# Optimization experiments

Hardware: AMD Instinct MI355X
Metric: run time of the kernel (lower is better)

## Reference

```python
import jax, jax.numpy as jnp
import numpy as np
import math

EPS = 1e-5
BN_SCALE = 1.0 / math.sqrt(1.0 + EPS)  # eval BatchNorm with running mean 0, var 1


def _ln(x, g, b):
    m = jnp.mean(x, axis=-1, keepdims=True)
    v = jnp.mean((x - m) ** 2, axis=-1, keepdims=True)
    return (x - m) * jax.lax.rsqrt(v + EPS) * g + b


def _swish(x):
    return x * jax.nn.sigmoid(x)


def _ffn(x, ng, nb, w1, b1, w2, b2):
    h = _ln(x, ng, nb)
    h = _swish(h @ w1.T + b1)
    return h @ w2.T + b2


def _mhsa(x, a_ng, a_nb, qkv_w, qkv_b, rel_w, out_w, out_b):
    B, T, D = x.shape
    H, hd = rel_w.shape  # rel_pos_proj: Linear(head_dim, num_heads), weight [H, hd]
    h = _ln(x, a_ng, a_nb)
    qkv = (h @ qkv_w.T + qkv_b).reshape(B, T, 3, H, hd)
    q = qkv[:, :, 0].transpose(0, 2, 1, 3)  # [B,H,T,hd]
    k = qkv[:, :, 1].transpose(0, 2, 1, 3)
    v = qkv[:, :, 2].transpose(0, 2, 1, 3)
    scores = jnp.einsum('bhqd,bhkd->bhqk', q, k) * (hd ** -0.5)
    # relative sinusoidal PE over 2T-1 offsets
    pos = jnp.arange(-(T - 1), T, dtype=x.dtype)[:, None]
    div = jnp.exp(jnp.arange(0, hd, 2, dtype=x.dtype) * (-math.log(10000.0) / hd))
    ang = pos * div  # [2T-1, hd/2]
    pe = jnp.zeros((2 * T - 1, hd), dtype=x.dtype)
    pe = pe.at[:, 0::2].set(jnp.sin(ang)).at[:, 1::2].set(jnp.cos(ang))
    rel_bias = pe @ rel_w.T  # [2T-1, H]
    idx = jnp.arange(T)[:, None] - jnp.arange(T)[None, :] + (T - 1)  # [T,T]
    bias = rel_bias[idx].transpose(2, 0, 1)  # [H,T,T]
    attn = jax.nn.softmax(scores + bias[None], axis=-1)
    o = jnp.einsum('bhqk,bhkd->bhqd', attn, v).transpose(0, 2, 1, 3).reshape(B, T, D)
    return o @ out_w.T + out_b


def _conv(x, c_ng, c_nb, pw1_w, pw1_b, dw_w, dw_b, bn_g, bn_b, pw2_w, pw2_b):
    B, T, D = x.shape
    K = dw_w.shape[1]
    h = _ln(x, c_ng, c_nb)
    h = h @ pw1_w.T + pw1_b  # pointwise conv == linear, [B,T,2D]
    a, g = jnp.split(h, 2, axis=-1)
    h = a * jax.nn.sigmoid(g)  # GLU, [B,T,D]
    h = h.transpose(0, 2, 1)  # [B,D,T]
    h = jax.lax.conv_general_dilated(
        h, dw_w[:, None, :], window_strides=(1,), padding=[(K // 2, K // 2)],
        dimension_numbers=('NCH', 'OIH', 'NCH'), feature_group_count=D) + dw_b[:, None]
    h = h * (BN_SCALE * bn_g)[:, None] + bn_b[:, None]  # eval-mode BatchNorm1d
    h = _swish(h)
    h = h.transpose(0, 2, 1)  # [B,T,D]
    return h @ pw2_w.T + pw2_b


def _forward(x, g_ffn1, b_ffn1, g_mhsa, b_mhsa, g_conv, b_conv, g_ffn2, b_ffn2, g_out, b_out,
             f1_ng, f1_nb, f1_w1, f1_b1, f1_w2, f1_b2,
             f2_ng, f2_nb, f2_w1, f2_b1, f2_w2, f2_b2,
             a_ng, a_nb, qkv_w, qkv_b, rel_w, out_w, out_b,
             c_ng, c_nb, pw1_w, pw1_b, dw_w, dw_b, bn_g, bn_b, pw2_w, pw2_b):
    x = x + 0.5 * _ffn(_ln(x, g_ffn1, b_ffn1), f1_ng, f1_nb, f1_w1, f1_b1, f1_w2, f1_b2)
    x = x + _mhsa(_ln(x, g_mhsa, b_mhsa), a_ng, a_nb, qkv_w, qkv_b, rel_w, out_w, out_b)
    x = x + _conv(_ln(x, g_conv, b_conv), c_ng, c_nb, pw1_w, pw1_b, dw_w, dw_b, bn_g, bn_b, pw2_w, pw2_b)
    x = _ln(x + 0.5 * _ffn(_ln(x, g_ffn2, b_ffn2), f2_ng, f2_nb, f2_w1, f2_b1, f2_w2, f2_b2), g_out, b_out)
    return x


def setup_inputs() -> dict:
    key = jax.random.key(0)
    B, T, D, H, F, K = 8, 2048, 256, 4, 1024, 31
    ks = iter(jax.random.split(key, 16))
    w = lambda shape, s: jax.random.normal(next(ks), shape, jnp.float32) * s
    d = {}
    d['x'] = w((B, T, D), 1.0)
    for n in ['g_ffn1', 'g_mhsa', 'g_conv', 'g_ffn2', 'g_out', 'f1_ng', 'f2_ng', 'a_ng', 'c_ng', 'bn_g']:
        d[n] = jnp.ones((D,), jnp.float32)
    for n in ['b_ffn1', 'b_mhsa', 'b_conv', 'b_ffn2', 'b_out', 'f1_nb', 'f2_nb', 'a_nb', 'c_nb', 'bn_b']:
        d[n] = jnp.zeros((D,), jnp.float32)
    d['f1_w1'] = w((F, D), 0.05); d['f1_b1'] = jnp.zeros((F,), jnp.float32)
    d['f1_w2'] = w((D, F), 0.03); d['f1_b2'] = jnp.zeros((D,), jnp.float32)
    d['f2_w1'] = w((F, D), 0.05); d['f2_b1'] = jnp.zeros((F,), jnp.float32)
    d['f2_w2'] = w((D, F), 0.03); d['f2_b2'] = jnp.zeros((D,), jnp.float32)
    d['qkv_w'] = w((3 * D, D), 0.05); d['qkv_b'] = jnp.zeros((3 * D,), jnp.float32)
    d['rel_w'] = w((H, D // H), 0.05)
    d['out_w'] = w((D, D), 0.05); d['out_b'] = jnp.zeros((D,), jnp.float32)
    d['pw1_w'] = w((2 * D, D), 0.05); d['pw1_b'] = jnp.zeros((2 * D,), jnp.float32)
    d['dw_w'] = w((D, K), 0.1); d['dw_b'] = jnp.zeros((D,), jnp.float32)
    d['pw2_w'] = w((D, D), 0.05); d['pw2_b'] = jnp.zeros((D,), jnp.float32)
    return d


def reference(x, g_ffn1, b_ffn1, g_mhsa, b_mhsa, g_conv, b_conv, g_ffn2, b_ffn2, g_out, b_out,
              f1_ng, f1_nb, f1_w1, f1_b1, f1_w2, f1_b2,
              f2_ng, f2_nb, f2_w1, f2_b1, f2_w2, f2_b2,
              a_ng, a_nb, qkv_w, qkv_b, rel_w, out_w, out_b,
              c_ng, c_nb, pw1_w, pw1_b, dw_w, dw_b, bn_g, bn_b, pw2_w, pw2_b):
    return _forward(x, g_ffn1, b_ffn1, g_mhsa, b_mhsa, g_conv, b_conv, g_ffn2, b_ffn2, g_out, b_out,
                    f1_ng, f1_nb, f1_w1, f1_b1, f1_w2, f1_b2,
                    f2_ng, f2_nb, f2_w1, f2_b1, f2_w2, f2_b2,
                    a_ng, a_nb, qkv_w, qkv_b, rel_w, out_w, out_b,
                    c_ng, c_nb, pw1_w, pw1_b, dw_w, dw_b, bn_g, bn_b, pw2_w, pw2_b)
```

## Files before the change

kernel.cpp:

```cpp
#include <hip/hip_runtime.h>
#include <math.h>


typedef _Float16 half8 __attribute__((ext_vector_type(8)));
typedef _Float16 half4v __attribute__((ext_vector_type(4)));
typedef float floatx4 __attribute__((ext_vector_type(4)));

#define LN_EPS 1e-5f
#define BN_SCALE 0.9999950000374996f
#define LOG2E 1.44269504f
#define QSCALE (0.125f * LOG2E)

__device__ __forceinline__ void async_copy16(const _Float16* g, _Float16* l) {
    __builtin_amdgcn_global_load_lds(
        (const __attribute__((address_space(1))) void*)g,
        (__attribute__((address_space(3))) void*)l, 16, 0, 0);
}

struct CastJobs { const float* s[7]; _Float16* d[7]; };
__global__ __launch_bounds__(256) void cast_all(CastJobs j) {
    int i = blockIdx.x * 256 + threadIdx.x;
    int seg, base;
    if (i < 1048576)      { seg = i >> 18; base = seg << 18; }
    else if (i < 1245184) { seg = 4; base = 1048576; }
    else if (i < 1310720) { seg = 5; base = 1245184; }
    else                  { seg = 6; base = 1310720; }
    j.d[seg][i - base] = (_Float16)j.s[seg][i - base];
}

__global__ __launch_bounds__(256) void cast_pw1_kernel(const float* __restrict__ w,
        const float* __restrict__ b, _Float16* __restrict__ wp, float* __restrict__ bp) {
    int i = blockIdx.x * 256 + threadIdx.x;
    int p = i >> 8, c = i & 255;
    int chunk = p >> 4, within = p & 15;
    int orig = ((chunk & 1) ? 256 : 0) + (chunk >> 1) * 16 + within;
    wp[i] = (_Float16)w[orig * 256 + c];
    if (c == 0) bp[p] = b[orig];
}

__global__ __launch_bounds__(256) void ln2_kernel(const float* __restrict__ x,
        const float* __restrict__ g1, const float* __restrict__ b1,
        const float* __restrict__ g2, const float* __restrict__ b2,
        _Float16* __restrict__ y) {
    int wave = threadIdx.x >> 6, lane = threadIdx.x & 63;
    size_t row = (size_t)blockIdx.x * 4 + wave;
    float4 v = ((const float4*)(x + row * 256))[lane];
    float s = v.x + v.y + v.z + v.w;
    float s2 = v.x * v.x + v.y * v.y + v.z * v.z + v.w * v.w;
    #pragma unroll
    for (int m = 1; m < 64; m <<= 1) { s += __shfl_xor(s, m, 64); s2 += __shfl_xor(s2, m, 64); }
    float mean = s * (1.f / 256.f);
    float var = s2 * (1.f / 256.f) - mean * mean;
    float rs = rsqrtf(var + LN_EPS);
    int c0 = lane * 4;
    float y0 = (v.x - mean) * rs * g1[c0 + 0] + b1[c0 + 0];
    float y1 = (v.y - mean) * rs * g1[c0 + 1] + b1[c0 + 1];
    float y2 = (v.z - mean) * rs * g1[c0 + 2] + b1[c0 + 2];
    float y3 = (v.w - mean) * rs * g1[c0 + 3] + b1[c0 + 3];
    float t = y0 + y1 + y2 + y3;
    float t2 = y0 * y0 + y1 * y1 + y2 * y2 + y3 * y3;
    #pragma unroll
    for (int m = 1; m < 64; m <<= 1) { t += __shfl_xor(t, m, 64); t2 += __shfl_xor(t2, m, 64); }
    float mean2 = t * (1.f / 256.f);
    float var2 = t2 * (1.f / 256.f) - mean2 * mean2;
    float rs2 = rsqrtf(var2 + LN_EPS);
    half4v o;
    o[0] = (_Float16)((y0 - mean2) * rs2 * g2[c0 + 0] + b2[c0 + 0]);
    o[1] = (_Float16)((y1 - mean2) * rs2 * g2[c0 + 1] + b2[c0 + 1]);
    o[2] = (_Float16)((y2 - mean2) * rs2 * g2[c0 + 2] + b2[c0 + 2]);
    o[3] = (_Float16)((y3 - mean2) * rs2 * g2[c0 + 3] + b2[c0 + 3]);
    *(half4v*)(y + row * 256 + c0) = o;
}

template <int EPI>
__global__ __launch_bounds__(256) void gemm128(
        const _Float16* __restrict__ A, const _Float16* __restrict__ W,
        const float* __restrict__ bias, _Float16* __restrict__ outh,
        _Float16* __restrict__ outv, int N, int K) {
    __shared__ _Float16 As[128 * 64];
    __shared__ _Float16 Ws[128 * 64];
    int tid = threadIdx.x, wave = tid >> 6, lane = tid & 63;
    int n0 = blockIdx.x * 128, m0 = blockIdx.y * 128;
    int wr = wave >> 1, wc = wave & 1;
    floatx4 acc[4][4] = {};
    int l15 = lane & 15, quad = lane >> 4;
    int srow = wave * 32 + (lane >> 3);
    int scg  = (lane & 7) ^ ((lane >> 3) & 7);
    const _Float16* Aptr = A + (size_t)(m0 + srow) * K + scg * 8;
    const _Float16* Wptr = W + (size_t)(n0 + srow) * K + scg * 8;
    _Float16* AsBase = As + wave * 32 * 64;
    _Float16* WsBase = Ws + wave * 32 * 64;
    int r7 = l15 & 7;
    for (int k0 = 0; k0 < K; k0 += 64) {
        __syncthreads();
        #pragma unroll
        for (int i = 0; i < 4; i++)
            async_copy16(Aptr + k0 + (size_t)i * 8 * K, AsBase + i * 8 * 64);
        #pragma unroll
        for (int i = 0; i < 4; i++)
            async_copy16(Wptr + k0 + (size_t)i * 8 * K, WsBase + i * 8 * 64);
        __syncthreads();
        #pragma unroll
        for (int ks = 0; ks < 2; ks++) {
            int cg = ((ks * 4 + quad) ^ r7) * 8;
            half8 a[4], b[4];
            #pragma unroll
            for (int i = 0; i < 4; i++)
                a[i] = *(const half8*)&As[(wr * 64 + i * 16 + l15) * 64 + cg];
            #pragma unroll
            for (int j = 0; j < 4; j++)
                b[j] = *(const half8*)&Ws[(wc * 64 + j * 16 + l15) * 64 + cg];
            #pragma unroll
            for (int i = 0; i < 4; i++)
                #pragma unroll
                for (int j = 0; j < 4; j++)
                    acc[i][j] = __builtin_amdgcn_mfma_f32_16x16x32_f16(a[i], b[j], acc[i][j], 0, 0, 0);
        }
    }
    #pragma unroll
    for (int i = 0; i < 4; i++) {
        int mrow = m0 + wr * 64 + i * 16 + quad * 4;
        if (EPI == 2) {
            #pragma unroll
            for (int jp = 0; jp < 2; jp++) {
                int j = 2 * jp;
                int Pa = n0 + wc * 64 + j * 16 + l15;
                float ba = bias[Pa], bg = bias[Pa + 16];
                int d = ((Pa >> 5) << 4) + l15;
                #pragma unroll
                for (int r = 0; r < 4; r++) {
                    float av = acc[i][j][r] + ba;
                    float gv = acc[i][j + 1][r] + bg;
                    outh[(size_t)(mrow + r) * 256 + d] = (_Float16)(av / (1.f + __expf(-gv)));
                }
            }
        } else if (EPI == 5) {
            float qs = (n0 < 256) ? QSCALE : 1.f;
            #pragma unroll
            for (int j = 0; j < 4; j++) {
                int n = n0 + wc * 64 + j * 16 + l15;
                float bv = bias[n];
                if (n0 < 512) {
                    #pragma unroll
                    for (int r = 0; r < 4; r++)
                        outh[(size_t)(mrow + r) * N + n] = (_Float16)((acc[i][j][r] + bv) * qs);
                } else {
                    int hv = (n - 512) >> 6, d = (n - 512) & 63;
                    int bb = m0 >> 11;
                    int t0 = (m0 & 2047) + wr * 64 + i * 16 + quad * 4;
                    half4v vv;
                    #pragma unroll
                    for (int r = 0; r < 4; r++) vv[r] = (_Float16)(acc[i][j][r] + bv);
                    *(half4v*)(outv + ((size_t)((bb * 4 + hv) * 64 + d)) * 2048 + t0) = vv;
                }
            }
        } else {
            #pragma unroll
            for (int j = 0; j < 4; j++) {
                int n = n0 + wc * 64 + j * 16 + l15;
                float bv = bias[n];
                #pragma unroll
                for (int r = 0; r < 4; r++) {
                    float c = acc[i][j][r] + bv;
                    outh[(size_t)(mrow + r) * N + n] = (_Float16)(c / (1.f + __expf(-c)));
                }
            }
        }
    }
}

template <int FIN>
__global__ __launch_bounds__(256) void gemm_row(
        const _Float16* __restrict__ A, const _Float16* __restrict__ W,
        const float* __restrict__ bias, const float* __restrict__ res, float alpha,
        float* __restrict__ xNext, _Float16* __restrict__ t16out,
        float* __restrict__ finalOut,
        const float* __restrict__ g1, const float* __restrict__ b1,
        const float* __restrict__ g2, const float* __restrict__ b2, int K) {
    __shared__ _Float16 As[64 * 64];
    __shared__ _Float16 Ws[256 * 64];
    __shared__ float red[4][64][2];
    int tid = threadIdx.x, wave = tid >> 6, lane = tid & 63;
    int l15 = lane & 15, quad = lane >> 4;
    int m0 = blockIdx.x * 64;
    int sgsw = (tid & 7) ^ ((tid >> 3) & 7);
    int r7 = l15 & 7;
    floatx4 acc[4][4] = {};
    for (int k0 = 0; k0 < K; k0 += 64) {
        __syncthreads();
        #pragma unroll
        for (int i = 0; i < 2; i++) {
            int idx = tid + 256 * i;
            async_copy16(A + (size_t)(m0 + (idx >> 3)) * K + k0 + sgsw * 8, As + idx * 8);
        }
        #pragma unroll
        for (int i = 0; i < 8; i++) {
            int idx = tid + 256 * i;
            async_copy16(W + (size_t)(idx >> 3) * K + k0 + sgsw * 8, Ws + idx * 8);
        }
        __syncthreads();
        #pragma unroll
        for (int ks = 0; ks < 2; ks++) {
            int cg = ((ks * 4 + quad) ^ r7) * 8;
            half8 a[4], b[4];
            #pragma unroll
            for (int i = 0; i < 4; i++)
                a[i] = *(const half8*)&As[(i * 16 + l15) * 64 + cg];
            #pragma unroll
            for (int j = 0; j < 4; j++)
                b[j] = *(const half8*)&Ws[(wave * 64 + j * 16 + l15) * 64 + cg];
            #pragma unroll
            for (int i = 0; i < 4; i++)
                #pragma unroll
                for (int j = 0; j < 4; j++)
                    acc[i][j] = __builtin_amdgcn_mfma_f32_16x16x32_f16(a[i], b[j], acc[i][j], 0, 0, 0);
        }
    }
    int col[4];
    float bv[4], gg1[4], bb1[4], gg2[4], bb2[4];
    #pragma unroll
    for (int j = 0; j < 4; j++) {
        col[j] = wave * 64 + j * 16 + l15;
        bv[j] = bias[col[j]];
        gg1[j] = g1[col[j]]; bb1[j] = b1[col[j]];
        if (FIN == 0) { gg2[j] = g2[col[j]]; bb2[j] = b2[col[j]]; }
    }
    #pragma unroll
    for (int i = 0; i < 4; i++)
        #pragma unroll
        for (int r = 0; r < 4; r++) {
            size_t m = m0 + i * 16 + quad * 4 + r;
            #pragma unroll
            for (int j = 0; j < 4; j++) {
                float xv = res[m * 256 + col[j]] + alpha * (acc[i][j][r] + bv[j]);
                acc[i][j][r] = xv;
                if (FIN == 0) xNext[m * 256 + col[j]] = xv;
            }
        }
    #pragma unroll
    for (int i = 0; i < 4; i++)
        #pragma unroll
        for (int r = 0; r < 4; r++) {
            float s1 = 0.f, s2 = 0.f;
            #pragma unroll
            for (int j = 0; j < 4; j++) { float v = acc[i][j][r]; s1 += v; s2 += v * v; }
            #pragma unroll
            for (int mm = 1; mm < 16; mm <<= 1) { s1 += __shfl_xor(s1, mm, 64); s2 += __shfl_xor(s2, mm, 64); }
            if (l15 == 0) { red[wave][i * 16 + quad * 4 + r][0] = s1; red[wave][i * 16 + quad * 4 + r][1] = s2; }
        }
    __syncthreads();
    float mean1[4][4], rs1[4][4];
    #pragma unroll
    for (int i = 0; i < 4; i++)
        #pragma unroll
        for (int r = 0; r < 4; r++) {
            int row = i * 16 + quad * 4 + r;
            float T1 = red[0][row][0] + red[1][row][0] + red[2][row][0] + red[3][row][0];
            float T2 = red[0][row][1] + red[1][row][1] + red[2][row][1] + red[3][row][1];
            float mn = T1 * (1.f / 256.f);
            mean1[i][r] = mn;
            rs1[i][r] = rsqrtf(T2 * (1.f / 256.f) - mn * mn + LN_EPS);
        }
    if (FIN == 1) {
        #pragma unroll
        for (int i = 0; i < 4; i++)
            #pragma unroll
            for (int r = 0; r < 4; r++) {
                size_t m = m0 + i * 16 + quad * 4 + r;
                #pragma unroll
                for (int j = 0; j < 4; j++)
                    finalOut[m * 256 + col[j]] =
                        (acc[i][j][r] - mean1[i][r]) * rs1[i][r] * gg1[j] + bb1[j];
            }
        return;
    }
    #pragma unroll
    for (int i = 0; i < 4; i++)
        #pragma unroll
        for (int r = 0; r < 4; r++)
            #pragma unroll
            for (int j = 0; j < 4; j++)
                acc[i][j][r] = (acc[i][j][r] - mean1[i][r]) * rs1[i][r] * gg1[j] + bb1[j];
    __syncthreads();
    #pragma unroll
    for (int i = 0; i < 4; i++)
        #pragma unroll
        for (int r = 0; r < 4; r++) {
            float s1 = 0.f, s2 = 0.f;
            #pragma unroll
            for (int j = 0; j < 4; j++) { float v = acc[i][j][r]; s1 += v; s2 += v * v; }
            #pragma unroll
            for (int mm = 1; mm < 16; mm <<= 1) { s1 += __shfl_xor(s1, mm, 64); s2 += __shfl_xor(s2, mm, 64); }
            if (l15 == 0) { red[wave][i * 16 + quad * 4 + r][0] = s1; red[wave][i * 16 + quad * 4 + r][1] = s2; }
        }
    __syncthreads();
    #pragma unroll
    for (int i = 0; i < 4; i++)
        #pragma unroll
        for (int r = 0; r < 4; r++) {
            int row = i * 16 + quad * 4 + r;
            float T1 = red[0][row][0] + red[1][row][0] + red[2][row][0] + red[3][row][0];
            float T2 = red[0][row][1] + red[1][row][1] + red[2][row][1] + red[3][row][1];
            float mn = T1 * (1.f / 256.f);
            float rs = rsqrtf(T2 * (1.f / 256.f) - mn * mn + LN_EPS);
            size_t m = m0 + row;
            #pragma unroll
            for (int j = 0; j < 4; j++)
                t16out[m * 256 + col[j]] =
                    (_Float16)((acc[i][j][r] - mn) * rs * gg2[j] + bb2[j]);
        }
}

__global__ __launch_bounds__(256) void relbias_kernel(const float* __restrict__ rel_w,
                                                      float* __restrict__ rb) {
    int i = blockIdx.x * 256 + threadIdx.x;
    if (i >= 4095 * 4) return;
    int p = i >> 2, h = i & 3;
    float pos = (float)(p - 2047);
    const float c = -logf(10000.f) / 64.f;
    float acc = 0.f;
    for (int k = 0; k < 32; k++) {
        float dv = expf((float)(2 * k) * c);
        float ang = pos * dv;
        acc += sinf(ang) * rel_w[h * 64 + 2 * k] + cosf(ang) * rel_w[h * 64 + 2 * k + 1];
    }
    rb[h * 4095 + p] = acc * LOG2E;
}

__global__ __launch_bounds__(256) void attn_kernel(const _Float16* __restrict__ qkv,
        const _Float16* __restrict__ vtg, const float* __restrict__ rb,
        float* __restrict__ opart, float* __restrict__ lpart) {
    const int T = 2048;
    int qt = blockIdx.x & 15, ksp = blockIdx.x >> 4, h = blockIdx.y, b = blockIdx.z;
    int tid = threadIdx.x, wave = tid >> 6, lane = tid & 63;
    __shared__ __align__(16) _Float16 PQ[128 * 72];
    __shared__ __align__(16) _Float16 Ks[64][72];
    __shared__ __align__(16) _Float16 Vt[64][72];
    __shared__ __align__(16) float bias4[4][192];
    auto Qs = (_Float16(*)[72])PQ;
    auto Ps = (_Float16(*)[32][72])PQ;

    int l15 = lane & 15, quad = lane >> 4, kq = quad * 8;
    size_t qrow0 = (size_t)b * T + qt * 128;
    #pragma unroll
    for (int i = 0; i < 4; i++) {
        int idx = tid + 256 * i, r = idx >> 3, sg = idx & 7;
        *(float4*)(&Qs[r][sg * 8]) = *(const float4*)(qkv + (qrow0 + r) * 768 + h * 64 + sg * 8);
    }
    __syncthreads();
    half8 qa[2][2];
    #pragma unroll
    for (int u = 0; u < 2; u++)
        #pragma unroll
        for (int ks = 0; ks < 2; ks++)
            qa[u][ks] = *(const half8*)(&Qs[u * 64 + wave * 16 + l15][ks * 32 + kq]);
    half8 ones;
    #pragma unroll
    for (int j = 0; j < 8; j++) ones[j] = (_Float16)1.f;

    floatx4 oacc[2][4] = {};
    floatx4 lacc[2] = {};
    const float* rbh = rb + h * 4095;
    const _Float16* vbase = vtg + ((size_t)(b * 4 + h)) * 64 * 2048;
    const _Float16* kbase = qkv + ((size_t)b * T) * 768 + 256 + h * 64;
    int cshift = (63 - l15) & 3;

    for (int kt = ksp * 16; kt < ksp * 16 + 16; kt++) {
        __syncthreads();
        #pragma unroll
        for (int i = 0; i < 2; i++) {
            int idx = tid + 256 * i, r = idx >> 3, sg = idx & 7;
            *(float4*)(&Ks[r][sg * 8]) = *(const float4*)(kbase + (size_t)(kt * 64 + r) * 768 + sg * 8);
            *(float4*)(&Vt[r][sg * 8]) = *(const float4*)(vbase + (size_t)r * 2048 + kt * 64 + sg * 8);
        }
        if (tid < 192) {
            int base = qt * 128 - kt * 64 + 1984;
            float v = rbh[min(base + tid, 4094)];
            #pragma unroll
            for (int c = 0; c < 4; c++) {
                int idx = tid - c;
                if (idx >= 0) bias4[c][idx] = v;
            }
        }
        __syncthreads();
        half8 kf[2][4];
        #pragma unroll
        for (int ks = 0; ks < 2; ks++)
            #pragma unroll
            for (int nt = 0; nt < 4; nt++)
                kf[ks][nt] = *(const half8*)(&Ks[nt * 16 + l15][ks * 32 + kq]);
        floatx4 s[2][4];
        #pragma unroll
        for (int u = 0; u < 2; u++)
            #pragma unroll
            for (int nt = 0; nt < 4; nt++) {
                int cb = u * 64 + wave * 16 + quad * 4 - (nt * 16 + l15) + 63;
                s[u][nt] = *(const floatx4*)&bias4[cshift][cb - cshift];
            }
        #pragma unroll
        for (int u = 0; u < 2; u++)
            #pragma unroll
            for (int ks = 0; ks < 2; ks++)
                #pragma unroll
                for (int nt = 0; nt < 4; nt++)
                    s[u][nt] = __builtin_amdgcn_mfma_f32_16x16x32_f16(qa[u][ks], kf[ks][nt], s[u][nt], 0, 0, 0);
        #pragma unroll
        for (int u = 0; u < 2; u++)
            #pragma unroll
            for (int nt = 0; nt < 4; nt++)
                #pragma unroll
                for (int r = 0; r < 4; r++)
                    Ps[wave][u * 16 + quad * 4 + r][nt * 16 + l15] =
                        (_Float16)__builtin_amdgcn_exp2f(fminf(s[u][nt][r], 15.86f));
        half8 vf[2][4];
        #pragma unroll
        for (int ks = 0; ks < 2; ks++)
            #pragma unroll
            for (int nt = 0; nt < 4; nt++)
                vf[ks][nt] = *(const half8*)(&Vt[nt * 16 + l15][ks * 32 + kq]);
        #pragma unroll
        for (int u = 0; u < 2; u++)
            #pragma unroll
            for (int ks = 0; ks < 2; ks++) {
                half8 pa = *(const half8*)(&Ps[wave][u * 16 + l15][ks * 32 + kq]);
                lacc[u] = __builtin_amdgcn_mfma_f32_16x16x32_f16(pa, ones, lacc[u], 0, 0, 0);
                #pragma unroll
                for (int nt = 0; nt < 4; nt++)
                    oacc[u][nt] = __builtin_amdgcn_mfma_f32_16x16x32_f16(pa, vf[ks][nt], oacc[u][nt], 0, 0, 0);
            }
    }
    float* obase = opart + (size_t)ksp * 16384 * 256;
    #pragma unroll
    for (int u = 0; u < 2; u++) {
        size_t orow0 = qrow0 + u * 64 + wave * 16 + quad * 4;
        #pragma unroll
        for (int r = 0; r < 4; r++)
            #pragma unroll
            for (int nt = 0; nt < 4; nt++)
                obase[(orow0 + r) * 256 + h * 64 + nt * 16 + l15] = oacc[u][nt][r];
        if (l15 == 0) {
            int q = qt * 128 + u * 64 + wave * 16 + quad * 4;
            float* lp = lpart + ksp * 65536 + ((b * 4 + h) << 11) + q;
            #pragma unroll
            for (int r = 0; r < 4; r++) lp[r] = lacc[u][r];
        }
    }
}

__global__ __launch_bounds__(256) void attn_combine(const float* __restrict__ opart,
        const float* __restrict__ lpart, _Float16* __restrict__ o16) {
    int wave = threadIdx.x >> 6, lane = threadIdx.x & 63;
    size_t row = (size_t)blockIdx.x * 4 + wave;
    int c0 = lane * 4;
    float4 a = ((const float4*)(opart + row * 256))[lane];
    float4 bq = ((const float4*)(opart + (size_t)16384 * 256 + row * 256))[lane];
    int b = (int)(row >> 11), q = (int)(row & 2047), h = c0 >> 6;
    int li = ((b * 4 + h) << 11) + q;
    float inv = 1.f / (lpart[li] + lpart[65536 + li]);
    half4v o;
    o[0] = (_Float16)((a.x + bq.x) * inv);
    o[1] = (_Float16)((a.y + bq.y) * inv);
    o[2] = (_Float16)((a.z + bq.z) * inv);
    o[3] = (_Float16)((a.w + bq.w) * inv);
    *(half4v*)(o16 + row * 256 + c0) = o;
}

__global__ __launch_bounds__(256) void dwconv_kernel(const _Float16* __restrict__ glu,
        const float* __restrict__ dw_w, const float* __restrict__ dw_b,
        const float* __restrict__ bn_g, const float* __restrict__ bn_b,
        _Float16* __restrict__ out) {
    const int T = 2048;
    int d = threadIdx.x;
    int b = blockIdx.y, t0 = blockIdx.x * 32;
    const _Float16* base = glu + ((size_t)b * T) * 256 + d;
    float w[31], win[31];
    #pragma unroll
    for (int j = 0; j < 31; j++) w[j] = dw_w[d * 31 + j];
    #pragma unroll
    for (int j = 0; j < 31; j++) {
        int tt = t0 - 15 + j;
        win[j] = (tt >= 0 && tt < T) ? (float)base[(size_t)tt * 256] : 0.f;
    }
    float dwb = dw_b[d];
    float bns = BN_SCALE * bn_g[d];
    float bnb = bn_b[d];
    size_t orow = ((size_t)b * T) * 256 + d;
    #pragma unroll
    for (int i = 0; i < 32; i += 4) {
        float nl[4];
        #pragma unroll
        for (int u = 0; u < 4; u++) {
            int tn = t0 + i + u + 16;
            nl[u] = (tn < T) ? (float)base[(size_t)tn * 256] : 0.f;
        }
        #pragma unroll
        for (int u = 0; u < 4; u++) {
            int t = t0 + i + u;
            float acc = dwb;
            #pragma unroll
            for (int j = 0; j < 31; j++) acc += win[j] * w[j];
            float bn = acc * bns + bnb;
            out[orow + (size_t)t * 256] = (_Float16)(bn / (1.f + __expf(-bn)));
            #pragma unroll
            for (int j = 0; j < 30; j++) win[j] = win[j + 1];
            win[30] = nl[u];
        }
    }
}

extern "C" void kernel_launch(void* const* d_in, const int* in_sizes, int n_in,
                              void* d_out, int out_size, void* d_ws, size_t ws_size,
                              hipStream_t stream) {
    (void)in_sizes; (void)n_in; (void)out_size; (void)ws_size;
    const float* x      = (const float*)d_in[0];
    const float* g_ffn1 = (const float*)d_in[1];
    const float* g_mhsa = (const float*)d_in[2];
    const float* g_conv = (const float*)d_in[3];
    const float* g_ffn2 = (const float*)d_in[4];
    const float* g_out  = (const float*)d_in[5];
    const float* f1_ng  = (const float*)d_in[6];
    const float* f2_ng  = (const float*)d_in[7];
    const float* a_ng   = (const float*)d_in[8];
    const float* c_ng   = (const float*)d_in[9];
    const float* bn_g   = (const float*)d_in[10];
    const float* b_ffn1 = (const float*)d_in[11];
    const float* b_mhsa = (const float*)d_in[12];
    const float* b_conv = (const float*)d_in[13];
    const float* b_ffn2 = (const float*)d_in[14];
    const float* b_out  = (const float*)d_in[15];
    const float* f1_nb  = (const float*)d_in[16];
    const float* f2_nb  = (const float*)d_in[17];
    const float* a_nb   = (const float*)d_in[18];
    const float* c_nb   = (const float*)d_in[19];
    const float* bn_b   = (const float*)d_in[20];
    const float* f1_w1  = (const float*)d_in[21];
    const float* f1_b1  = (const float*)d_in[22];
    const float* f1_w2  = (const float*)d_in[23];
    const float* f1_b2  = (const float*)d_in[24];
    const float* f2_w1  = (const float*)d_in[25];
    const float* f2_b1  = (const float*)d_in[26];
    const float* f2_w2  = (const float*)d_in[27];
    const float* f2_b2  = (const float*)d_in[28];
    const float* qkv_w  = (const float*)d_in[29];
    const float* qkv_b  = (const float*)d_in[30];
    const float* rel_w  = (const float*)d_in[31];
    const float* out_w  = (const float*)d_in[32];
    const float* out_b  = (const float*)d_in[33];
    const float* pw1_w  = (const float*)d_in[34];
    const float* pw1_b  = (const float*)d_in[35];
    const float* dw_w   = (const float*)d_in[36];
    const float* dw_b   = (const float*)d_in[37];
    const float* pw2_w  = (const float*)d_in[38];
    const float* pw2_b  = (const float*)d_in[39];

    const int BT = 16384;
    char* ws = (char*)d_ws;
    size_t off = 0;
    auto alloc = [&](size_t bytes) -> char* {
        char* p = ws + off;
        off += (bytes + 255) & ~(size_t)255;
        return p;
    };
    _Float16* wf1w1 = (_Float16*)alloc(262144 * 2);
    _Float16* wf1w2 = (_Float16*)alloc(262144 * 2);
    _Float16* wf2w1 = (_Float16*)alloc(262144 * 2);
    _Float16* wf2w2 = (_Float16*)alloc(262144 * 2);
    _Float16* wqkv  = (_Float16*)alloc(196608 * 2);
    _Float16* wout  = (_Float16*)alloc(65536 * 2);
    _Float16* wpw1  = (_Float16*)alloc(131072 * 2);
    float* pb1      = (float*)alloc(512 * 4);
    _Float16* wpw2  = (_Float16*)alloc(65536 * 2);
    float* rbbuf    = (float*)alloc(4 * 4095 * 4);
    float* xA       = (float*)alloc((size_t)BT * 256 * 4);
    float* xB       = (float*)alloc((size_t)BT * 256 * 4);
    _Float16* t16   = (_Float16*)alloc((size_t)BT * 256 * 2);
    char* R1        = alloc((size_t)BT * 1024 * 2);
    _Float16* vtg   = (_Float16*)alloc((size_t)8 * 4 * 64 * 2048 * 2);
    float* opart    = (float*)alloc((size_t)2 * BT * 256 * 4);
    float* lpart    = (float*)alloc((size_t)2 * 65536 * 4);
    _Float16* glu16 = (_Float16*)alloc((size_t)BT * 256 * 2);
    _Float16* c16   = (_Float16*)alloc((size_t)BT * 256 * 2);
    _Float16* o16   = (_Float16*)alloc((size_t)BT * 256 * 2);
    _Float16* h16   = (_Float16*)R1;
    _Float16* qkv16 = (_Float16*)R1;

    CastJobs cj;
    cj.s[0] = f1_w1; cj.d[0] = wf1w1;
    cj.s[1] = f1_w2; cj.d[1] = wf1w2;
    cj.s[2] = f2_w1; cj.d[2] = wf2w1;
    cj.s[3] = f2_w2; cj.d[3] = wf2w2;
    cj.s[4] = qkv_w; cj.d[4] = wqkv;
    cj.s[5] = out_w; cj.d[5] = wout;
    cj.s[6] = pw2_w; cj.d[6] = wpw2;
    cast_all<<<5376, 256, 0, stream>>>(cj);
    cast_pw1_kernel<<<512, 256, 0, stream>>>(pw1_w, pw1_b, wpw1, pb1);
    relbias_kernel<<<64, 256, 0, stream>>>(rel_w, rbbuf);

    ln2_kernel<<<BT / 4, 256, 0, stream>>>(x, g_ffn1, b_ffn1, f1_ng, f1_nb, t16);
    gemm128<1><<<dim3(8, 128), 256, 0, stream>>>(t16, wf1w1, f1_b1, h16, nullptr, 1024, 256);
    gemm_row<0><<<256, 256, 0, stream>>>(h16, wf1w2, f1_b2, x, 0.5f, xA, t16, nullptr,
                                         g_mhsa, b_mhsa, a_ng, a_nb, 1024);
    gemm128<5><<<dim3(6, 128), 256, 0, stream>>>(t16, wqkv, qkv_b, qkv16, vtg, 768, 256);
    attn_kernel<<<dim3(32, 4, 8), 256, 0, stream>>>(qkv16, vtg, rbbuf, opart, lpart);
    attn_combine<<<BT / 4, 256, 0, stream>>>(opart, lpart, o16);
    gemm_row<0><<<256, 256, 0, stream>>>(o16, wout, out_b, xA, 1.f, xB, t16, nullptr,
                                         g_conv, b_conv, c_ng, c_nb, 256);
    gemm128<2><<<dim3(4, 128), 256, 0, stream>>>(t16, wpw1, pb1, glu16, nullptr, 512, 256);
    dwconv_kernel<<<dim3(64, 8), 256, 0, stream>>>(glu16, dw_w, dw_b, bn_g, bn_b, c16);
    gemm_row<0><<<256, 256, 0, stream>>>(c16, wpw2, pw2_b, xB, 1.f, xA, t16, nullptr,
                                         g_ffn2, b_ffn2, f2_ng, f2_nb, 256);
    gemm128<1><<<dim3(8, 128), 256, 0, stream>>>(t16, wf2w1, f2_b1, h16, nullptr, 1024, 256);
    gemm_row<1><<<256, 256, 0, stream>>>(h16, wf2w2, f2_b2, xA, 0.5f, nullptr, nullptr,
                                         (float*)d_out, g_out, b_out, nullptr, nullptr, 1024);
}
```

Before: 486.4 us.

## Drop attention split-K combine, shrink row-GEMM tiles to 32 rows

The attention kernel no longer splits the key range into two partial passes written as fp32 partials and merged by a separate combine kernel. Each block now owns 64 queries over all 2048 keys and writes normalized fp16 output directly, and K/V/Q tiles are loaded with async global-to-LDS copies. The LayerNorm-fused row GEMM goes from 64-row to 32-row tiles, doubling its grid to 512 blocks for better CU occupancy. The trade-offs are more redundant weight-tile loads per row in the GEMM and a longer serial key loop per attention block, plus an unpadded LDS layout that may cause bank conflicts.

```diff
diff --git a/kernel.cpp b/kernel.cpp
--- a/kernel.cpp
+++ b/kernel.cpp
@@ -177,22 +177,18 @@
         float* __restrict__ finalOut,
         const float* __restrict__ g1, const float* __restrict__ b1,
         const float* __restrict__ g2, const float* __restrict__ b2, int K) {
-    __shared__ _Float16 As[64 * 64];
+    __shared__ _Float16 As[32 * 64];
     __shared__ _Float16 Ws[256 * 64];
-    __shared__ float red[4][64][2];
+    __shared__ float red[4][32][2];
     int tid = threadIdx.x, wave = tid >> 6, lane = tid & 63;
     int l15 = lane & 15, quad = lane >> 4;
-    int m0 = blockIdx.x * 64;
+    int m0 = blockIdx.x * 32;
     int sgsw = (tid & 7) ^ ((tid >> 3) & 7);
     int r7 = l15 & 7;
-    floatx4 acc[4][4] = {};
+    floatx4 acc[2][4] = {};
     for (int k0 = 0; k0 < K; k0 += 64) {
         __syncthreads();
-        #pragma unroll
-        for (int i = 0; i < 2; i++) {
-            int idx = tid + 256 * i;
-            async_copy16(A + (size_t)(m0 + (idx >> 3)) * K + k0 + sgsw * 8, As + idx * 8);
-        }
+        async_copy16(A + (size_t)(m0 + (tid >> 3)) * K + k0 + sgsw * 8, As + tid * 8);
         #pragma unroll
         for (int i = 0; i < 8; i++) {
             int idx = tid + 256 * i;
@@ -202,15 +198,15 @@
         #pragma unroll
         for (int ks = 0; ks < 2; ks++) {
             int cg = ((ks * 4 + quad) ^ r7) * 8;
-            half8 a[4], b[4];
-            #pragma unroll
-            for (int i = 0; i < 4; i++)
+            half8 a[2], b[4];
+            #pragma unroll
+            for (int i = 0; i < 2; i++)
                 a[i] = *(const half8*)&As[(i * 16 + l15) * 64 + cg];
             #pragma unroll
             for (int j = 0; j < 4; j++)
                 b[j] = *(const half8*)&Ws[(wave * 64 + j * 16 + l15) * 64 + cg];
             #pragma unroll
-            for (int i = 0; i < 4; i++)
+            for (int i = 0; i < 2; i++)
                 #pragma unroll
                 for (int j = 0; j < 4; j++)
                     acc[i][j] = __builtin_amdgcn_mfma_f32_16x16x32_f16(a[i], b[j], acc[i][j], 0, 0, 0);
@@ -226,7 +222,7 @@
         if (FIN == 0) { gg2[j] = g2[col[j]]; bb2[j] = b2[col[j]]; }
     }
     #pragma unroll
-    for (int i = 0; i < 4; i++)
+    for (int i = 0; i < 2; i++)
         #pragma unroll
         for (int r = 0; r < 4; r++) {
             size_t m = m0 + i * 16 + quad * 4 + r;
@@ -238,7 +234,7 @@
             }
         }
     #pragma unroll
-    for (int i = 0; i < 4; i++)
+    for (int i = 0; i < 2; i++)
         #pragma unroll
         for (int r = 0; r < 4; r++) {
             float s1 = 0.f, s2 = 0.f;
@@ -249,9 +245,9 @@
             if (l15 == 0) { red[wave][i * 16 + quad * 4 + r][0] = s1; red[wave][i * 16 + quad * 4 + r][1] = s2; }
         }
     __syncthreads();
-    float mean1[4][4], rs1[4][4];
-    #pragma unroll
-    for (int i = 0; i < 4; i++)
+    float mean1[2][4], rs1[2][4];
+    #pragma unroll
+    for (int i = 0; i < 2; i++)
         #pragma unroll
         for (int r = 0; r < 4; r++) {
             int row = i * 16 + quad * 4 + r;
@@ -263,7 +259,7 @@
         }
     if (FIN == 1) {
         #pragma unroll
-        for (int i = 0; i < 4; i++)
+        for (int i = 0; i < 2; i++)
             #pragma unroll
             for (int r = 0; r < 4; r++) {
                 size_t m = m0 + i * 16 + quad * 4 + r;
@@ -275,7 +271,7 @@
         return;
     }
     #pragma unroll
-    for (int i = 0; i < 4; i++)
+    for (int i = 0; i < 2; i++)
         #pragma unroll
         for (int r = 0; r < 4; r++)
             #pragma unroll
@@ -283,7 +279,7 @@
                 acc[i][j][r] = (acc[i][j][r] - mean1[i][r]) * rs1[i][r] * gg1[j] + bb1[j];
     __syncthreads();
     #pragma unroll
-    for (int i = 0; i < 4; i++)
+    for (int i = 0; i < 2; i++)
         #pragma unroll
         for (int r = 0; r < 4; r++) {
             float s1 = 0.f, s2 = 0.f;
@@ -295,7 +291,7 @@
         }
     __syncthreads();
     #pragma unroll
-    for (int i = 0; i < 4; i++)
+    for (int i = 0; i < 2; i++)
         #pragma unroll
         for (int r = 0; r < 4; r++) {
             int row = i * 16 + quad * 4 + r;
@@ -329,52 +325,50 @@
 
 __global__ __launch_bounds__(256) void attn_kernel(const _Float16* __restrict__ qkv,
         const _Float16* __restrict__ vtg, const float* __restrict__ rb,
-        float* __restrict__ opart, float* __restrict__ lpart) {
+        _Float16* __restrict__ o16) {
     const int T = 2048;
-    int qt = blockIdx.x & 15, ksp = blockIdx.x >> 4, h = blockIdx.y, b = blockIdx.z;
+    int qt = blockIdx.x, h = blockIdx.y, b = blockIdx.z;
     int tid = threadIdx.x, wave = tid >> 6, lane = tid & 63;
-    __shared__ __align__(16) _Float16 PQ[128 * 72];
-    __shared__ __align__(16) _Float16 Ks[64][72];
-    __shared__ __align__(16) _Float16 Vt[64][72];
-    __shared__ __align__(16) float bias4[4][192];
-    auto Qs = (_Float16(*)[72])PQ;
-    auto Ps = (_Float16(*)[32][72])PQ;
+    __shared__ __align__(16) _Float16 PQ[4608];
+    __shared__ __align__(16) _Float16 Ks[64 * 64];
+    __shared__ __align__(16) _Float16 Vt[64 * 64];
+    __shared__ __align__(16) float bias4[4][136];
+    _Float16* Qs = PQ;
+    auto Ps = (_Float16(*)[16][72])PQ;
 
     int l15 = lane & 15, quad = lane >> 4, kq = quad * 8;
-    size_t qrow0 = (size_t)b * T + qt * 128;
-    #pragma unroll
-    for (int i = 0; i < 4; i++) {
-        int idx = tid + 256 * i, r = idx >> 3, sg = idx & 7;
-        *(float4*)(&Qs[r][sg * 8]) = *(const float4*)(qkv + (qrow0 + r) * 768 + h * 64 + sg * 8);
+    size_t qrow0 = (size_t)b * T + qt * 64;
+    #pragma unroll
+    for (int i = 0; i < 2; i++) {
+        int idx = tid + 256 * i;
+        async_copy16(qkv + (qrow0 + (idx >> 3)) * 768 + h * 64 + (idx & 7) * 8, PQ + idx * 8);
     }
     __syncthreads();
-    half8 qa[2][2];
-    #pragma unroll
-    for (int u = 0; u < 2; u++)
-        #pragma unroll
-        for (int ks = 0; ks < 2; ks++)
-            qa[u][ks] = *(const half8*)(&Qs[u * 64 + wave * 16 + l15][ks * 32 + kq]);
+    half8 qa[2];
+    #pragma unroll
+    for (int ks = 0; ks < 2; ks++)
+        qa[ks] = *(const half8*)&Qs[(wave * 16 + l15) * 64 + ks * 32 + kq];
     half8 ones;
     #pragma unroll
     for (int j = 0; j < 8; j++) ones[j] = (_Float16)1.f;
 
-    floatx4 oacc[2][4] = {};
-    floatx4 lacc[2] = {};
+    floatx4 oacc[4] = {};
+    floatx4 lacc = {};
     const float* rbh = rb + h * 4095;
     const _Float16* vbase = vtg + ((size_t)(b * 4 + h)) * 64 * 2048;
     const _Float16* kbase = qkv + ((size_t)b * T) * 768 + 256 + h * 64;
     int cshift = (63 - l15) & 3;
 
-    for (int kt = ksp * 16; kt < ksp * 16 + 16; kt++) {
+    for (int kt = 0; kt < 32; kt++) {
         __syncthreads();
         #pragma unroll
         for (int i = 0; i < 2; i++) {
-            int idx = tid + 256 * i, r = idx >> 3, sg = idx & 7;
-            *(float4*)(&Ks[r][sg * 8]) = *(const float4*)(kbase + (size_t)(kt * 64 + r) * 768 + sg * 8);
-            *(float4*)(&Vt[r][sg * 8]) = *(const float4*)(vbase + (size_t)r * 2048 + kt * 64 + sg * 8);
-        }
-        if (tid < 192) {
-            int base = qt * 128 - kt * 64 + 1984;
+            int idx = tid + 256 * i, row = idx >> 3, cg = idx & 7;
+            async_copy16(kbase + (size_t)(kt * 64 + row) * 768 + cg * 8, Ks + idx * 8);
+            async_copy16(vbase + (size_t)row * 2048 + kt * 64 + cg * 8, Vt + idx * 8);
+        }
+        if (tid < 136) {
+            int base = qt * 64 - kt * 64 + 1984;
             float v = rbh[min(base + tid, 4094)];
             #pragma unroll
             for (int c = 0; c < 4; c++) {
@@ -388,81 +382,47 @@
         for (int ks = 0; ks < 2; ks++)
             #pragma unroll
             for (int nt = 0; nt < 4; nt++)
-                kf[ks][nt] = *(const half8*)(&Ks[nt * 16 + l15][ks * 32 + kq]);
-        floatx4 s[2][4];
-        #pragma unroll
-        for (int u = 0; u < 2; u++)
-            #pragma unroll
-            for (int nt = 0; nt < 4; nt++) {
-                int cb = u * 64 + wave * 16 + quad * 4 - (nt * 16 + l15) + 63;
-                s[u][nt] = *(const floatx4*)&bias4[cshift][cb - cshift];
-            }
-        #pragma unroll
-        for (int u = 0; u < 2; u++)
-            #pragma unroll
-            for (int ks = 0; ks < 2; ks++)
-                #pragma unroll
-                for (int nt = 0; nt < 4; nt++)
-                    s[u][nt] = __builtin_amdgcn_mfma_f32_16x16x32_f16(qa[u][ks], kf[ks][nt], s[u][nt], 0, 0, 0);
-        #pragma unroll
-        for (int u = 0; u < 2; u++)
+                kf[ks][nt] = *(const half8*)&Ks[(nt * 16 + l15) * 64 + ks * 32 + kq];
+        floatx4 s[4];
+        #pragma unroll
+        for (int nt = 0; nt < 4; nt++) {
+            int cb = wave * 16 + quad * 4 - (nt * 16 + l15) + 63;
+            s[nt] = *(const floatx4*)&bias4[cshift][cb - cshift];
+        }
+        #pragma unroll
+        for (int ks = 0; ks < 2; ks++)
             #pragma unroll
             for (int nt = 0; nt < 4; nt++)
-                #pragma unroll
-                for (int r = 0; r < 4; r++)
-                    Ps[wave][u * 16 + quad * 4 + r][nt * 16 + l15] =
-                        (_Float16)__builtin_amdgcn_exp2f(fminf(s[u][nt][r], 15.86f));
+                s[nt] = __builtin_amdgcn_mfma_f32_16x16x32_f16(qa[ks], kf[ks][nt], s[nt], 0, 0, 0);
+        #pragma unroll
+        for (int nt = 0; nt < 4; nt++)
+            #pragma unroll
+            for (int r = 0; r < 4; r++)
+                Ps[wave][quad * 4 + r][nt * 16 + l15] =
+                    (_Float16)__builtin_amdgcn_exp2f(fminf(s[nt][r], 15.86f));
         half8 vf[2][4];
         #pragma unroll
         for (int ks = 0; ks < 2; ks++)
             #pragma unroll
             for (int nt = 0; nt < 4; nt++)
-                vf[ks][nt] = *(const half8*)(&Vt[nt * 16 + l15][ks * 32 + kq]);
-        #pragma unroll
-        for (int u = 0; u < 2; u++)
-            #pragma unroll
-            for (int ks = 0; ks < 2; ks++) {
-                half8 pa = *(const half8*)(&Ps[wave][u * 16 + l15][ks * 32 + kq]);
-                lacc[u] = __builtin_amdgcn_mfma_f32_16x16x32_f16(pa, ones, lacc[u], 0, 0, 0);
-                #pragma unroll
-                for (int nt = 0; nt < 4; nt++)
-                    oacc[u][nt] = __builtin_amdgcn_mfma_f32_16x16x32_f16(pa, vf[ks][nt], oacc[u][nt], 0, 0, 0);
-            }
-    }
-    float* obase = opart + (size_t)ksp * 16384 * 256;
-    #pragma unroll
-    for (int u = 0; u < 2; u++) {
-        size_t orow0 = qrow0 + u * 64 + wave * 16 + quad * 4;
-        #pragma unroll
-        for (int r = 0; r < 4; r++)
+                vf[ks][nt] = *(const half8*)&Vt[(nt * 16 + l15) * 64 + ks * 32 + kq];
+        #pragma unroll
+        for (int ks = 0; ks < 2; ks++) {
+            half8 pa = *(const half8*)&Ps[wave][l15][ks * 32 + kq];
+            lacc = __builtin_amdgcn_mfma_f32_16x16x32_f16(pa, ones, lacc, 0, 0, 0);
             #pragma unroll
             for (int nt = 0; nt < 4; nt++)
-                obase[(orow0 + r) * 256 + h * 64 + nt * 16 + l15] = oacc[u][nt][r];
-        if (l15 == 0) {
-            int q = qt * 128 + u * 64 + wave * 16 + quad * 4;
-            float* lp = lpart + ksp * 65536 + ((b * 4 + h) << 11) + q;
-            #pragma unroll
-            for (int r = 0; r < 4; r++) lp[r] = lacc[u][r];
-        }
-    }
-}
-
-__global__ __launch_bounds__(256) void attn_combine(const float* __restrict__ opart,
-        const float* __restrict__ lpart, _Float16* __restrict__ o16) {
-    int wave = threadIdx.x >> 6, lane = threadIdx.x & 63;
-    size_t row = (size_t)blockIdx.x * 4 + wave;
-    int c0 = lane * 4;
-    float4 a = ((const float4*)(opart + row * 256))[lane];
-    float4 bq = ((const float4*)(opart + (size_t)16384 * 256 + row * 256))[lane];
-    int b = (int)(row >> 11), q = (int)(row & 2047), h = c0 >> 6;
-    int li = ((b * 4 + h) << 11) + q;
-    float inv = 1.f / (lpart[li] + lpart[65536 + li]);
-    half4v o;
-    o[0] = (_Float16)((a.x + bq.x) * inv);
-    o[1] = (_Float16)((a.y + bq.y) * inv);
-    o[2] = (_Float16)((a.z + bq.z) * inv);
-    o[3] = (_Float16)((a.w + bq.w) * inv);
-    *(half4v*)(o16 + row * 256 + c0) = o;
+                oacc[nt] = __builtin_amdgcn_mfma_f32_16x16x32_f16(pa, vf[ks][nt], oacc[nt], 0, 0, 0);
+        }
+    }
+    size_t orow0 = qrow0 + wave * 16 + quad * 4;
+    #pragma unroll
+    for (int r = 0; r < 4; r++) {
+        float inv = 1.f / lacc[r];
+        #pragma unroll
+        for (int nt = 0; nt < 4; nt++)
+            o16[(orow0 + r) * 256 + h * 64 + nt * 16 + l15] = (_Float16)(oacc[nt][r] * inv);
+    }
 }
 
 __global__ __launch_bounds__(256) void dwconv_kernel(const _Float16* __restrict__ glu,
@@ -576,8 +536,6 @@
     _Float16* t16   = (_Float16*)alloc((size_t)BT * 256 * 2);
     char* R1        = alloc((size_t)BT * 1024 * 2);
     _Float16* vtg   = (_Float16*)alloc((size_t)8 * 4 * 64 * 2048 * 2);
-    float* opart    = (float*)alloc((size_t)2 * BT * 256 * 4);
-    float* lpart    = (float*)alloc((size_t)2 * 65536 * 4);
     _Float16* glu16 = (_Float16*)alloc((size_t)BT * 256 * 2);
     _Float16* c16   = (_Float16*)alloc((size_t)BT * 256 * 2);
     _Float16* o16   = (_Float16*)alloc((size_t)BT * 256 * 2);
@@ -598,18 +556,17 @@
 
     ln2_kernel<<<BT / 4, 256, 0, stream>>>(x, g_ffn1, b_ffn1, f1_ng, f1_nb, t16);
     gemm128<1><<<dim3(8, 128), 256, 0, stream>>>(t16, wf1w1, f1_b1, h16, nullptr, 1024, 256);
-    gemm_row<0><<<256, 256, 0, stream>>>(h16, wf1w2, f1_b2, x, 0.5f, xA, t16, nullptr,
+    gemm_row<0><<<512, 256, 0, stream>>>(h16, wf1w2, f1_b2, x, 0.5f, xA, t16, nullptr,
                                          g_mhsa, b_mhsa, a_ng, a_nb, 1024);
     gemm128<5><<<dim3(6, 128), 256, 0, stream>>>(t16, wqkv, qkv_b, qkv16, vtg, 768, 256);
-    attn_kernel<<<dim3(32, 4, 8), 256, 0, stream>>>(qkv16, vtg, rbbuf, opart, lpart);
-    attn_combine<<<BT / 4, 256, 0, stream>>>(opart, lpart, o16);
-    gemm_row<0><<<256, 256, 0, stream>>>(o16, wout, out_b, xA, 1.f, xB, t16, nullptr,
+    attn_kernel<<<dim3(32, 4, 8), 256, 0, stream>>>(qkv16, vtg, rbbuf, o16);
+    gemm_row<0><<<512, 256, 0, stream>>>(o16, wout, out_b, xA, 1.f, xB, t16, nullptr,
                                          g_conv, b_conv, c_ng, c_nb, 256);
     gemm128<2><<<dim3(4, 128), 256, 0, stream>>>(t16, wpw1, pb1, glu16, nullptr, 512, 256);
     dwconv_kernel<<<dim3(64, 8), 256, 0, stream>>>(glu16, dw_w, dw_b, bn_g, bn_b, c16);
-    gemm_row<0><<<256, 256, 0, stream>>>(c16, wpw2, pw2_b, xB, 1.f, xA, t16, nullptr,
+    gemm_row<0><<<512, 256, 0, stream>>>(c16, wpw2, pw2_b, xB, 1.f, xA, t16, nullptr,
                                          g_ffn2, b_ffn2, f2_ng, f2_nb, 256);
     gemm128<1><<<dim3(8, 128), 256, 0, stream>>>(t16, wf2w1, f2_b1, h16, nullptr, 1024, 256);
-    gemm_row<1><<<256, 256, 0, stream>>>(h16, wf2w2, f2_b2, xA, 0.5f, nullptr, nullptr,
+    gemm_row<1><<<512, 256, 0, stream>>>(h16, wf2w2, f2_b2, xA, 0.5f, nullptr, nullptr,
                                          (float*)d_out, g_out, b_out, nullptr, nullptr, 1024);
 }
```

Result: faster. 455.1 us (-6.4%).
